# Performance work log

Measured on AMD Instinct MI355X. Metric: run time of the kernel, lower is better.

Reference implementation:

```python
import jax, jax.numpy as jnp
import numpy as np

T = 4096
MOL = 2048
DESC = 6
NSOL = 5
H = 2048
D_BLOCK = MOL + DESC            # 2054
FUSE = D_BLOCK * (1 + NSOL)     # 12324
D_IN = FUSE + 1                 # 12325
BOUNDARY_RF = 0.5
CLAMP_LO, CLAMP_HI = 1e-4, 1.0 - 1e-4


def setup_inputs() -> dict:
    key = jax.random.key(0)
    ks = jax.random.split(key, 32)
    s = 0.02  # weight init scale for numerical stability
    d = {
        "mol_vec": jax.random.normal(ks[0], (MOL,), jnp.float32),
        "solvent_seq": jax.random.uniform(ks[1], (T, NSOL), jnp.float32),
        "desc_seq": jax.random.normal(ks[2], (T, DESC), jnp.float32),
        "rf_true": jax.random.uniform(ks[3], (T,), jnp.float32),
        "solvent_vecs": jax.random.normal(ks[4], (NSOL, MOL), jnp.float32),
    }
    wshapes = [
        ("Wf0", (H, D_IN)), ("Wf1", (H, H)), ("Wf2", (H, H)), ("Wof", (1, H)),
        ("Wb0", (H, D_IN)), ("Wb1", (H, H)), ("Wb2", (H, H)), ("Wob", (1, H)),
    ]
    for i, (name, shp) in enumerate(wshapes):
        d[name] = jax.random.normal(ks[5 + i], shp, jnp.float32) * s
    for name, shp in [("bf0", (H,)), ("bf1", (H,)), ("bf2", (H,)), ("bof", (1,)),
                      ("bb0", (H,)), ("bb1", (H,)), ("bb2", (H,)), ("bob", (1,))]:
        d[name] = jnp.zeros(shp, jnp.float32)
    return d


def _step_features(mol_vec, solvent_seq, desc_seq, solvent_vecs):
    # mol_vec [MOL]; solvent_seq [T,NSOL]; desc_seq [T,DESC]; solvent_vecs [NSOL,MOL]
    mol_cat = jnp.concatenate(
        [jnp.broadcast_to(mol_vec, (T, MOL)), desc_seq], axis=-1)  # [T, D_BLOCK]
    scaled = solvent_seq[:, :, None] * solvent_vecs[None, :, :]      # [T,NSOL,MOL]
    sol_block = jnp.concatenate(
        [scaled, jnp.broadcast_to(desc_seq[:, None, :], (T, NSOL, DESC))], axis=-1)
    sol_flat = sol_block.reshape(T, NSOL * D_BLOCK)
    return jnp.concatenate([mol_cat, sol_flat], axis=-1)             # [T, FUSE]


def _trunk(x, W0, b0, W1, b1, W2, b2):
    # 3 Linear+GELU blocks (dropout is identity in eval)
    h = jax.nn.gelu(x @ W0.T + b0, approximate=False)
    h = jax.nn.gelu(h @ W1.T + b1, approximate=False)
    h = jax.nn.gelu(h @ W2.T + b2, approximate=False)
    return h


def reference(mol_vec, solvent_seq, desc_seq, rf_true, solvent_vecs,
              Wf0, bf0, Wf1, bf1, Wf2, bf2, Wof, bof,
              Wb0, bb0, Wb1, bb1, Wb2, bb2, Wob, bob):
    x = _step_features(mol_vec, solvent_seq, desc_seq, solvent_vecs)  # [T, FUSE]
    rf = jax.lax.stop_gradient(rf_true)  # teacher signal is detached
    b = jnp.asarray([BOUNDARY_RF], dtype=x.dtype)
    prev = jnp.concatenate([b, rf[:-1]])  # fwd branch sees rf_true[t-1]
    nxt = jnp.concatenate([rf[1:], b])    # bwd branch sees rf_true[t+1]

    inp_f = jnp.concatenate([x, prev[:, None]], axis=-1)  # [T, D_IN]
    inp_b = jnp.concatenate([x, nxt[:, None]], axis=-1)

    hf = _trunk(inp_f, Wf0, bf0, Wf1, bf1, Wf2, bf2)
    hb = _trunk(inp_b, Wb0, bb0, Wb1, bb1, Wb2, bb2)
    rf_fwd = (hf @ Wof.T + bof).squeeze(-1)  # [T]
    rf_bwd = (hb @ Wob.T + bob).squeeze(-1)
    rf_fwd = jnp.clip(rf_fwd, CLAMP_LO, CLAMP_HI)
    rf_bwd = jnp.clip(rf_bwd, CLAMP_LO, CLAMP_HI)
    return rf_fwd, rf_bwd
```

## Files before the change

kernel.cpp:

```cpp
#include <hip/hip_runtime.h>
#include <hip/hip_fp16.h>
#include <math.h>

#define T_DIM 4096
#define MOL_N 2048
#define DESC_N 6
#define NSOL_N 5
#define H_DIM 2048
#define DBLK 2054
#define D_IN_N 12325

typedef _Float16 f16x8 __attribute__((ext_vector_type(8)));
typedef float f32x4 __attribute__((ext_vector_type(4)));

__device__ __forceinline__ float gelu_f(float x) {
    float v = x * (1.5957691f + 0.0713548f * x * x);
    float e = __expf(-v);
    return x / (1.0f + e);
}

__global__ __launch_bounds__(256) void fold_kernel(
    const float* __restrict__ W0f, const float* __restrict__ W0b,
    const float* __restrict__ b0f, const float* __restrict__ b0b,
    const float* __restrict__ mol, const float* __restrict__ sv,
    float* __restrict__ fold_f, float* __restrict__ fold_b)
{
    const int h = blockIdx.x;
    const int z = blockIdx.y;
    const float* __restrict__ W0 = z ? W0b : W0f;
    const float* __restrict__ b0 = z ? b0b : b0f;
    float* __restrict__ fold = z ? fold_b : fold_f;
    const float* __restrict__ row = W0 + (size_t)h * D_IN_N;
    const int tid = threadIdx.x;

    float acc[6] = {0.f, 0.f, 0.f, 0.f, 0.f, 0.f};
    for (int c = tid; c < MOL_N; c += 256) {
        float m = mol[c];
        acc[0] += row[c] * m;
        #pragma unroll
        for (int s = 0; s < NSOL_N; ++s)
            acc[1 + s] += row[DBLK * (s + 1) + c] * sv[s * MOL_N + c];
    }
    #pragma unroll
    for (int i = 0; i < 6; ++i) {
        float v = acc[i];
        #pragma unroll
        for (int off = 32; off >= 1; off >>= 1)
            v += __shfl_xor(v, off, 64);
        acc[i] = v;
    }
    __shared__ float red[4][6];
    const int lane = tid & 63, wave = tid >> 6;
    if (lane == 0) {
        #pragma unroll
        for (int i = 0; i < 6; ++i) red[wave][i] = acc[i];
    }
    __syncthreads();
    if (tid < 6) {
        float s = red[0][tid] + red[1][tid] + red[2][tid] + red[3][tid];
        if (tid == 0) fold[h] = s + b0[h];
        else fold[(size_t)tid * H_DIM + h] = s;
    }
    if (tid >= 64 && tid < 70) {
        int j = tid - 64;
        float w = row[MOL_N + j];
        #pragma unroll
        for (int s = 0; s < NSOL_N; ++s) w += row[DBLK * (s + 1) + MOL_N + j];
        fold[(size_t)(6 + j) * H_DIM + h] = w;
    }
    if (tid == 70) fold[(size_t)12 * H_DIM + h] = row[D_IN_N - 1];
}

__global__ __launch_bounds__(256) void conv_kernel(
    const float* __restrict__ W1f, const float* __restrict__ W2f,
    const float* __restrict__ W1b, const float* __restrict__ W2b,
    _Float16* __restrict__ dstbase)
{
    const int z = blockIdx.y;
    const float* __restrict__ src = (z == 0) ? W1f : (z == 1) ? W2f : (z == 2) ? W1b : W2b;
    _Float16* __restrict__ dst = dstbase + (size_t)z * H_DIM * H_DIM;
    const int idx = blockIdx.x * 256 + threadIdx.x;
    float4 v = ((const float4*)src)[idx];
    struct h4 { _Float16 a, b, c, d; };
    h4 o;
    o.a = (_Float16)v.x; o.b = (_Float16)v.y; o.c = (_Float16)v.z; o.d = (_Float16)v.w;
    ((h4*)dst)[idx] = o;
}

__global__ __launch_bounds__(256) void h0_kernel(
    const float* __restrict__ fold_f, const float* __restrict__ fold_b,
    const float* __restrict__ desc, const float* __restrict__ sol,
    const float* __restrict__ rf,
    _Float16* __restrict__ h0f, _Float16* __restrict__ h0b)
{
    const int z = blockIdx.z;
    const float* __restrict__ fold = z ? fold_b : fold_f;
    _Float16* __restrict__ h0 = z ? h0b : h0f;
    const int h = blockIdx.x * 256 + threadIdx.x;
    const int tbase = blockIdx.y * 64;

    const float c0 = fold[h];
    float u[NSOL_N], wd[DESC_N];
    #pragma unroll
    for (int s = 0; s < NSOL_N; ++s) u[s] = fold[(size_t)(1 + s) * H_DIM + h];
    #pragma unroll
    for (int j = 0; j < DESC_N; ++j) wd[j] = fold[(size_t)(6 + j) * H_DIM + h];
    const float wp = fold[(size_t)12 * H_DIM + h];

    for (int i = 0; i < 64; ++i) {
        const int t = tbase + i;
        float pv;
        if (z == 0) pv = (t == 0) ? 0.5f : rf[t - 1];
        else        pv = (t == T_DIM - 1) ? 0.5f : rf[t + 1];
        float pre = c0 + wp * pv;
        #pragma unroll
        for (int s = 0; s < NSOL_N; ++s) pre += u[s] * sol[t * NSOL_N + s];
        #pragma unroll
        for (int j = 0; j < DESC_N; ++j) pre += wd[j] * desc[t * DESC_N + j];
        h0[(size_t)t * H_DIM + h] = (_Float16)gelu_f(pre);
    }
}

__global__ __launch_bounds__(256) void gemm_kernel(
    const _Float16* __restrict__ Af, const _Float16* __restrict__ Ab,
    const _Float16* __restrict__ Wfp, const _Float16* __restrict__ Wbp,
    const float* __restrict__ bfp, const float* __restrict__ bbp,
    _Float16* __restrict__ Cf, _Float16* __restrict__ Cb)
{
    constexpr int K = H_DIM;
    constexpr int N = H_DIM;
    const int bid = blockIdx.x;
    const int xcd = bid & 7;
    const int slot = bid >> 3;
    const int z = xcd & 1;
    const int q = xcd >> 1;
    const int m0 = (q * 8 + (slot & 7)) * 128;
    const int n0 = (slot >> 3) * 128;

    const _Float16* __restrict__ A = z ? Ab : Af;
    const _Float16* __restrict__ W = z ? Wbp : Wfp;
    const float* __restrict__ bias = z ? bbp : bfp;
    _Float16* __restrict__ C = z ? Cb : Cf;

    __shared__ _Float16 sA[128 * 64];
    __shared__ _Float16 sB[128 * 64];

    const int tid = threadIdx.x;
    const int wave = tid >> 6;
    const int lane = tid & 63;
    const int quad = lane >> 4;

    char* sAc = (char*)sA;
    char* sBc = (char*)sB;

    const _Float16* gA[4];
    const _Float16* gB[4];
    #pragma unroll
    for (int ld = 0; ld < 4; ++ld) {
        const int j = ld * 256 + tid;
        const int r = j >> 3;
        const int c = (j & 7) ^ (r & 7);
        gA[ld] = A + (size_t)(m0 + r) * K + c * 8;
        gB[ld] = W + (size_t)(n0 + r) * K + c * 8;
    }

    f32x4 acc[4][4];
    #pragma unroll
    for (int i = 0; i < 4; ++i)
        #pragma unroll
        for (int j = 0; j < 4; ++j)
            acc[i][j] = (f32x4){0.f, 0.f, 0.f, 0.f};

    const int rA = (wave & 1) * 64 + (lane & 15);
    const int rB = (wave >> 1) * 64 + (lane & 15);
    const int xorL = lane & 7;

    for (int k0 = 0; k0 < K; k0 += 64) {
        #pragma unroll
        for (int ld = 0; ld < 4; ++ld)
            __builtin_amdgcn_global_load_lds(
                (const __attribute__((address_space(1))) void*)(gA[ld] + k0),
                (__attribute__((address_space(3))) void*)(sAc + ld * 4096 + wave * 1024), 16, 0, 0);
        #pragma unroll
        for (int ld = 0; ld < 4; ++ld)
            __builtin_amdgcn_global_load_lds(
                (const __attribute__((address_space(1))) void*)(gB[ld] + k0),
                (__attribute__((address_space(3))) void*)(sBc + ld * 4096 + wave * 1024), 16, 0, 0);
        __syncthreads();
        #pragma unroll
        for (int kk = 0; kk < 2; ++kk) {
            const int coff = ((kk * 4 + quad) ^ xorL) * 16;
            f16x8 aF[4], bF[4];
            #pragma unroll
            for (int mi = 0; mi < 4; ++mi)
                aF[mi] = *(const f16x8*)(sAc + (rA + mi * 16) * 128 + coff);
            #pragma unroll
            for (int ni = 0; ni < 4; ++ni)
                bF[ni] = *(const f16x8*)(sBc + (rB + ni * 16) * 128 + coff);
            #pragma unroll
            for (int mi = 0; mi < 4; ++mi)
                #pragma unroll
                for (int ni = 0; ni < 4; ++ni)
                    acc[mi][ni] = __builtin_amdgcn_mfma_f32_16x16x32_f16(aF[mi], bF[ni], acc[mi][ni], 0, 0, 0);
        }
        __syncthreads();
    }

    const int colC = lane & 15;
    #pragma unroll
    for (int ni = 0; ni < 4; ++ni) {
        const int n = n0 + (wave >> 1) * 64 + ni * 16 + colC;
        const float bv = bias[n];
        #pragma unroll
        for (int mi = 0; mi < 4; ++mi) {
            const int mb = m0 + (wave & 1) * 64 + mi * 16 + quad * 4;
            #pragma unroll
            for (int r = 0; r < 4; ++r) {
                float v = acc[mi][ni][r] + bv;
                C[(size_t)(mb + r) * N + n] = (_Float16)gelu_f(v);
            }
        }
    }
}

__global__ __launch_bounds__(256) void out_kernel(
    const _Float16* __restrict__ h2f, const _Float16* __restrict__ h2b,
    const float* __restrict__ Wof, const float* __restrict__ Wob,
    const float* __restrict__ bof, const float* __restrict__ bob,
    float* __restrict__ out)
{
    const int t = blockIdx.x;
    const int z = blockIdx.y;
    const _Float16* __restrict__ h2 = z ? h2b : h2f;
    const float* __restrict__ Wo = z ? Wob : Wof;
    const float bo = z ? bob[0] : bof[0];
    const int tid = threadIdx.x;
    const int c = tid * 8;
    const f16x8 hv = *(const f16x8*)(h2 + (size_t)t * H_DIM + c);
    float acc = 0.f;
    #pragma unroll
    for (int j = 0; j < 8; ++j)
        acc += (float)hv[j] * Wo[c + j];
    #pragma unroll
    for (int off = 32; off >= 1; off >>= 1)
        acc += __shfl_xor(acc, off, 64);
    __shared__ float red[4];
    const int lane = tid & 63, wave = tid >> 6;
    if (lane == 0) red[wave] = acc;
    __syncthreads();
    if (tid == 0) {
        float v = red[0] + red[1] + red[2] + red[3] + bo;
        v = fminf(fmaxf(v, 1e-4f), 1.0f - 1e-4f);
        out[(size_t)z * T_DIM + t] = v;
    }
}

extern "C" void kernel_launch(void* const* d_in, const int* in_sizes, int n_in,
                              void* d_out, int out_size, void* d_ws, size_t ws_size,
                              hipStream_t stream)
{
    (void)in_sizes; (void)n_in; (void)out_size; (void)ws_size;
    const float* mol = (const float*)d_in[0];
    const float* sol = (const float*)d_in[1];
    const float* desc = (const float*)d_in[2];
    const float* rf  = (const float*)d_in[3];
    const float* sv  = (const float*)d_in[4];
    const float* Wf0 = (const float*)d_in[5];
    const float* Wf1 = (const float*)d_in[6];
    const float* Wf2 = (const float*)d_in[7];
    const float* Wof = (const float*)d_in[8];
    const float* Wb0 = (const float*)d_in[9];
    const float* Wb1 = (const float*)d_in[10];
    const float* Wb2 = (const float*)d_in[11];
    const float* Wob = (const float*)d_in[12];
    const float* bf0 = (const float*)d_in[13];
    const float* bf1 = (const float*)d_in[14];
    const float* bf2 = (const float*)d_in[15];
    const float* bof = (const float*)d_in[16];
    const float* bb0 = (const float*)d_in[17];
    const float* bb1 = (const float*)d_in[18];
    const float* bb2 = (const float*)d_in[19];
    const float* bob = (const float*)d_in[20];
    float* out = (float*)d_out;

    char* ws = (char*)d_ws;
    float* fold_f = (float*)(ws + 0);
    float* fold_b = (float*)(ws + 131072);
    _Float16* Wc = (_Float16*)(ws + 262144);
    const size_t WSZ = (size_t)H_DIM * H_DIM;
    _Float16* W1f_c = Wc;
    _Float16* W2f_c = Wc + WSZ;
    _Float16* W1b_c = Wc + 2 * WSZ;
    _Float16* W2b_c = Wc + 3 * WSZ;
    const size_t HSZ = (size_t)T_DIM * H_DIM;
    _Float16* h0f = (_Float16*)(ws + 33816576);
    _Float16* h0b = h0f + HSZ;
    _Float16* h1f = (_Float16*)(ws + 33816576 + 2 * 16777216);
    _Float16* h1b = h1f + HSZ;
    _Float16* h2f = h0f;
    _Float16* h2b = h0b;

    fold_kernel<<<dim3(H_DIM, 2), 256, 0, stream>>>(Wf0, Wb0, bf0, bb0, mol, sv, fold_f, fold_b);
    conv_kernel<<<dim3(H_DIM * H_DIM / 1024, 4), 256, 0, stream>>>(Wf1, Wf2, Wb1, Wb2, Wc);
    h0_kernel<<<dim3(8, 64, 2), 256, 0, stream>>>(fold_f, fold_b, desc, sol, rf, h0f, h0b);
    gemm_kernel<<<dim3(1024), 256, 0, stream>>>(h0f, h0b, W1f_c, W1b_c, bf1, bb1, h1f, h1b);
    gemm_kernel<<<dim3(1024), 256, 0, stream>>>(h1f, h1b, W2f_c, W2b_c, bf2, bb2, h2f, h2b);
    out_kernel<<<dim3(T_DIM, 2), 256, 0, stream>>>(h2f, h2b, Wof, Wob, bof, bob, out);
}
```

Baseline: 503.6 us.

## Fuse output projection into second hidden GEMM epilogue with atomic accumulation

The third GEMM's epilogue now applies GELU and immediately dots each tile with the output weight vector, reducing across lanes and atomically adding partial sums into a small float buffer. This removes the fp16 write and re-read of the final hidden activations and the separate out_kernel. A memset and a tiny finalize kernel are added to apply the output bias and clamp. The fold loop is also fully unrolled. Float atomics make the summation order nondeterministic.

```diff
diff --git a/kernel.cpp b/kernel.cpp
--- a/kernel.cpp
+++ b/kernel.cpp
@@ -34,8 +34,10 @@
     const int tid = threadIdx.x;
 
     float acc[6] = {0.f, 0.f, 0.f, 0.f, 0.f, 0.f};
-    for (int c = tid; c < MOL_N; c += 256) {
-        float m = mol[c];
+    #pragma unroll
+    for (int i = 0; i < 8; ++i) {
+        const int c = tid + i * 256;
+        const float m = mol[c];
         acc[0] += row[c] * m;
         #pragma unroll
         for (int s = 0; s < NSOL_N; ++s)
@@ -223,36 +225,129 @@
     }
 }
 
-__global__ __launch_bounds__(256) void out_kernel(
-    const _Float16* __restrict__ h2f, const _Float16* __restrict__ h2b,
+__global__ __launch_bounds__(256) void gemm_out_kernel(
+    const _Float16* __restrict__ Af, const _Float16* __restrict__ Ab,
+    const _Float16* __restrict__ Wfp, const _Float16* __restrict__ Wbp,
+    const float* __restrict__ bfp, const float* __restrict__ bbp,
     const float* __restrict__ Wof, const float* __restrict__ Wob,
+    float* __restrict__ out_acc)
+{
+    constexpr int K = H_DIM;
+    const int bid = blockIdx.x;
+    const int xcd = bid & 7;
+    const int slot = bid >> 3;
+    const int z = xcd & 1;
+    const int q = xcd >> 1;
+    const int m0 = (q * 8 + (slot & 7)) * 128;
+    const int n0 = (slot >> 3) * 128;
+
+    const _Float16* __restrict__ A = z ? Ab : Af;
+    const _Float16* __restrict__ W = z ? Wbp : Wfp;
+    const float* __restrict__ bias = z ? bbp : bfp;
+    const float* __restrict__ Wo = z ? Wob : Wof;
+
+    __shared__ _Float16 sA[128 * 64];
+    __shared__ _Float16 sB[128 * 64];
+
+    const int tid = threadIdx.x;
+    const int wave = tid >> 6;
+    const int lane = tid & 63;
+    const int quad = lane >> 4;
+
+    char* sAc = (char*)sA;
+    char* sBc = (char*)sB;
+
+    const _Float16* gA[4];
+    const _Float16* gB[4];
+    #pragma unroll
+    for (int ld = 0; ld < 4; ++ld) {
+        const int j = ld * 256 + tid;
+        const int r = j >> 3;
+        const int c = (j & 7) ^ (r & 7);
+        gA[ld] = A + (size_t)(m0 + r) * K + c * 8;
+        gB[ld] = W + (size_t)(n0 + r) * K + c * 8;
+    }
+
+    f32x4 acc[4][4];
+    #pragma unroll
+    for (int i = 0; i < 4; ++i)
+        #pragma unroll
+        for (int j = 0; j < 4; ++j)
+            acc[i][j] = (f32x4){0.f, 0.f, 0.f, 0.f};
+
+    const int rA = (wave & 1) * 64 + (lane & 15);
+    const int rB = (wave >> 1) * 64 + (lane & 15);
+    const int xorL = lane & 7;
+
+    for (int k0 = 0; k0 < K; k0 += 64) {
+        #pragma unroll
+        for (int ld = 0; ld < 4; ++ld)
+            __builtin_amdgcn_global_load_lds(
+                (const __attribute__((address_space(1))) void*)(gA[ld] + k0),
+                (__attribute__((address_space(3))) void*)(sAc + ld * 4096 + wave * 1024), 16, 0, 0);
+        #pragma unroll
+        for (int ld = 0; ld < 4; ++ld)
+            __builtin_amdgcn_global_load_lds(
+                (const __attribute__((address_space(1))) void*)(gB[ld] + k0),
+                (__attribute__((address_space(3))) void*)(sBc + ld * 4096 + wave * 1024), 16, 0, 0);
+        __syncthreads();
+        #pragma unroll
+        for (int kk = 0; kk < 2; ++kk) {
+            const int coff = ((kk * 4 + quad) ^ xorL) * 16;
+            f16x8 aF[4], bF[4];
+            #pragma unroll
+            for (int mi = 0; mi < 4; ++mi)
+                aF[mi] = *(const f16x8*)(sAc + (rA + mi * 16) * 128 + coff);
+            #pragma unroll
+            for (int ni = 0; ni < 4; ++ni)
+                bF[ni] = *(const f16x8*)(sBc + (rB + ni * 16) * 128 + coff);
+            #pragma unroll
+            for (int mi = 0; mi < 4; ++mi)
+                #pragma unroll
+                for (int ni = 0; ni < 4; ++ni)
+                    acc[mi][ni] = __builtin_amdgcn_mfma_f32_16x16x32_f16(aF[mi], bF[ni], acc[mi][ni], 0, 0, 0);
+        }
+        __syncthreads();
+    }
+
+    const int colC = lane & 15;
+    float bv[4], wo[4];
+    #pragma unroll
+    for (int ni = 0; ni < 4; ++ni) {
+        const int n = n0 + (wave >> 1) * 64 + ni * 16 + colC;
+        bv[ni] = bias[n];
+        wo[ni] = Wo[n];
+    }
+    #pragma unroll
+    for (int mi = 0; mi < 4; ++mi) {
+        #pragma unroll
+        for (int r = 0; r < 4; ++r) {
+            float s = 0.f;
+            #pragma unroll
+            for (int ni = 0; ni < 4; ++ni)
+                s += gelu_f(acc[mi][ni][r] + bv[ni]) * wo[ni];
+            s += __shfl_xor(s, 1, 64);
+            s += __shfl_xor(s, 2, 64);
+            s += __shfl_xor(s, 4, 64);
+            s += __shfl_xor(s, 8, 64);
+            if (colC == 0) {
+                const int row = m0 + (wave & 1) * 64 + mi * 16 + quad * 4 + r;
+                atomicAdd(&out_acc[z * T_DIM + row], s);
+            }
+        }
+    }
+}
+
+__global__ __launch_bounds__(256) void finalize_kernel(
+    const float* __restrict__ out_acc,
     const float* __restrict__ bof, const float* __restrict__ bob,
     float* __restrict__ out)
 {
-    const int t = blockIdx.x;
-    const int z = blockIdx.y;
-    const _Float16* __restrict__ h2 = z ? h2b : h2f;
-    const float* __restrict__ Wo = z ? Wob : Wof;
-    const float bo = z ? bob[0] : bof[0];
-    const int tid = threadIdx.x;
-    const int c = tid * 8;
-    const f16x8 hv = *(const f16x8*)(h2 + (size_t)t * H_DIM + c);
-    float acc = 0.f;
-    #pragma unroll
-    for (int j = 0; j < 8; ++j)
-        acc += (float)hv[j] * Wo[c + j];
-    #pragma unroll
-    for (int off = 32; off >= 1; off >>= 1)
-        acc += __shfl_xor(acc, off, 64);
-    __shared__ float red[4];
-    const int lane = tid & 63, wave = tid >> 6;
-    if (lane == 0) red[wave] = acc;
-    __syncthreads();
-    if (tid == 0) {
-        float v = red[0] + red[1] + red[2] + red[3] + bo;
-        v = fminf(fmaxf(v, 1e-4f), 1.0f - 1e-4f);
-        out[(size_t)z * T_DIM + t] = v;
-    }
+    const int idx = blockIdx.x * 256 + threadIdx.x;
+    const int z = idx >> 12;
+    float v = out_acc[idx] + (z ? bob[0] : bof[0]);
+    v = fminf(fmaxf(v, 1e-4f), 1.0f - 1e-4f);
+    out[idx] = v;
 }
 
 extern "C" void kernel_launch(void* const* d_in, const int* in_sizes, int n_in,
@@ -297,13 +392,13 @@
     _Float16* h0b = h0f + HSZ;
     _Float16* h1f = (_Float16*)(ws + 33816576 + 2 * 16777216);
     _Float16* h1b = h1f + HSZ;
-    _Float16* h2f = h0f;
-    _Float16* h2b = h0b;
+    float* out_acc = (float*)(ws + 33816576);
 
     fold_kernel<<<dim3(H_DIM, 2), 256, 0, stream>>>(Wf0, Wb0, bf0, bb0, mol, sv, fold_f, fold_b);
     conv_kernel<<<dim3(H_DIM * H_DIM / 1024, 4), 256, 0, stream>>>(Wf1, Wf2, Wb1, Wb2, Wc);
     h0_kernel<<<dim3(8, 64, 2), 256, 0, stream>>>(fold_f, fold_b, desc, sol, rf, h0f, h0b);
     gemm_kernel<<<dim3(1024), 256, 0, stream>>>(h0f, h0b, W1f_c, W1b_c, bf1, bb1, h1f, h1b);
-    gemm_kernel<<<dim3(1024), 256, 0, stream>>>(h1f, h1b, W2f_c, W2b_c, bf2, bb2, h2f, h2b);
-    out_kernel<<<dim3(T_DIM, 2), 256, 0, stream>>>(h2f, h2b, Wof, Wob, bof, bob, out);
-}
+    hipMemsetAsync(out_acc, 0, 2 * T_DIM * sizeof(float), stream);
+    gemm_out_kernel<<<dim3(1024), 256, 0, stream>>>(h1f, h1b, W2f_c, W2b_c, bf2, bb2, Wof, Wob, out_acc);
+    finalize_kernel<<<dim3(2 * T_DIM / 256), 256, 0, stream>>>(out_acc, bof, bob, out);
+}
```

New measurement: 488.1 us. 3.1% less time.
